# Optimization experiments

Measured on AMD Instinct MI355X. Metric: run time of the kernel, lower is better.

Reference implementation:

```python
import jax, jax.numpy as jnp
import numpy as np

N = 100000
E = 3200000
NFEAT, NHID, NCLASS = 512, 256, 64
K = 10
ALPHA = 0.1


def setup_inputs() -> dict:
    key = jax.random.key(0)
    k1, k2, k3, k4, k5 = jax.random.split(key, 5)
    x = jax.random.normal(k1, (N, NFEAT), dtype=jnp.float32)
    edge_index = jax.random.randint(k2, (2, E), 0, N, dtype=jnp.int64)
    # Linear params (Kaiming-ish scale)
    W1 = jax.random.normal(k3, (NFEAT, NHID), dtype=jnp.float32) / np.sqrt(NFEAT)
    b1 = jnp.zeros((NHID,), dtype=jnp.float32)
    W2 = jax.random.normal(k4, (NHID, NCLASS), dtype=jnp.float32) / np.sqrt(NHID)
    b2 = jnp.zeros((NCLASS,), dtype=jnp.float32)
    # GPR coefficients: temp[k] = alpha*(1-alpha)^k, temp[K] = (1-alpha)^K
    temp = ALPHA * (1.0 - ALPHA) ** np.arange(K + 1)
    temp[-1] = (1.0 - ALPHA) ** K
    temp = jnp.asarray(temp, dtype=jnp.float32)
    return {"x": x, "edge_index": edge_index, "W1": W1, "b1": b1,
            "W2": W2, "b2": b2, "temp": temp}


def _gcn_norm(edge_index, num_nodes):
    # add self-loops, symmetric GCN normalization (PyG gcn_norm, edge_weight=1)
    loop = jnp.arange(num_nodes, dtype=edge_index.dtype)
    src = jnp.concatenate([edge_index[0], loop])
    dst = jnp.concatenate([edge_index[1], loop])
    deg = jnp.zeros((num_nodes,), dtype=jnp.float32).at[dst].add(1.0)
    dinv = jnp.where(deg > 0, jax.lax.rsqrt(deg), 0.0)
    norm = dinv[src] * dinv[dst]
    return src, dst, norm


def reference(x, edge_index, W1, b1, W2, b2, temp):
    n = x.shape[0]
    # eval mode: dropout is identity
    h = jax.nn.relu(x @ W1 + b1)
    h = h @ W2 + b2  # [N, nclass]
    src, dst, norm = _gcn_norm(edge_index, n)
    hidden = h * temp[0]
    for k in range(K):
        # one GCN-normalized hop: out[dst] += norm * h[src]
        h = jax.ops.segment_sum(norm[:, None] * h[src], dst, num_segments=n)
        hidden = hidden + temp[k + 1] * h
    return jax.nn.log_softmax(hidden, axis=1)
```

## Files before the change

### kernel.cpp

```cpp
#include <hip/hip_runtime.h>

#define N_NODES 100000
#define N_EDGES 3200000
#define NFEAT 512
#define NHID 256
#define NCLASS 64
#define KHOPS 10
#define SCAN_B 391

#define NBSHIFT 9
#define NBUCK 196
#define BCAP 20480
#define TILE 4096

typedef __bf16 bf16x8 __attribute__((ext_vector_type(8)));
typedef __bf16 bf16x4 __attribute__((ext_vector_type(4)));
typedef float f32x4 __attribute__((ext_vector_type(4)));


__global__ __launch_bounds__(256) void zero_deg_kernel(int* __restrict__ deg, int* __restrict__ bcursor) {
    int i = blockIdx.x * 256 + threadIdx.x;
    if (i < N_NODES) deg[i] = 0;
    if (blockIdx.x == 0 && threadIdx.x < NBUCK) bcursor[threadIdx.x] = 0;
}

__global__ __launch_bounds__(256) void deg_kernel(const int* __restrict__ ei, int* __restrict__ deg) {
    int e = blockIdx.x * 256 + threadIdx.x;
    if (e < N_EDGES) atomicAdd(&deg[ei[N_EDGES + e]], 1);
}

__global__ __launch_bounds__(256) void dinv_kernel(const int* __restrict__ deg, float* __restrict__ dinv) {
    int i = blockIdx.x * 256 + threadIdx.x;
    if (i < N_NODES) dinv[i] = rsqrtf((float)(deg[i] + 1));
}


__global__ __launch_bounds__(256) void scan1_kernel(const int* __restrict__ deg, int* __restrict__ partial) {
    __shared__ int red[256];
    int t = threadIdx.x;
    int i = blockIdx.x * 256 + t;
    red[t] = (i < N_NODES) ? deg[i] + 1 : 0;
    __syncthreads();
    for (int off = 128; off > 0; off >>= 1) {
        if (t < off) red[t] += red[t + off];
        __syncthreads();
    }
    if (t == 0) partial[blockIdx.x] = red[0];
}

__global__ __launch_bounds__(512) void scan2_kernel(int* __restrict__ partial) {
    __shared__ int s[512];
    int t = threadIdx.x;
    int v = (t < SCAN_B) ? partial[t] : 0;
    s[t] = v;
    __syncthreads();
    for (int off = 1; off < 512; off <<= 1) {
        int add = (t >= off) ? s[t - off] : 0;
        __syncthreads();
        s[t] += add;
        __syncthreads();
    }
    if (t < SCAN_B) partial[t] = s[t] - v;
}

__global__ __launch_bounds__(256) void scan3_kernel(const int* __restrict__ deg,
                                                    const int* __restrict__ partial,
                                                    int* __restrict__ row_ptr,
                                                    int* __restrict__ cursor) {
    __shared__ int s[256];
    int t = threadIdx.x;
    int i = blockIdx.x * 256 + t;
    int v = (i < N_NODES) ? deg[i] + 1 : 0;
    s[t] = v;
    __syncthreads();
    for (int off = 1; off < 256; off <<= 1) {
        int add = (t >= off) ? s[t - off] : 0;
        __syncthreads();
        s[t] += add;
        __syncthreads();
    }
    int excl = s[t] - v + partial[blockIdx.x];
    if (i < N_NODES) {
        row_ptr[i] = excl;
        cursor[i] = excl;
        if (i == N_NODES - 1) row_ptr[N_NODES] = excl + v;
    }
}


__global__ __launch_bounds__(256) void radix1_kernel(const int* __restrict__ ei,
                                                     int* __restrict__ bcursor,
                                                     int2* __restrict__ breg) {
    __shared__ int2 stage[TILE];
    __shared__ int hist[NBUCK];
    __shared__ int base[NBUCK];
    __shared__ int offs[NBUCK];
    int t = threadIdx.x;
    int e0 = blockIdx.x * TILE;
    int n = N_EDGES - e0; if (n > TILE) n = TILE;
    for (int i = t; i < NBUCK; i += 256) { hist[i] = 0; offs[i] = 0; }
    __syncthreads();
    for (int i = t; i < n; i += 256) {
        int s = ei[e0 + i];
        int d = ei[N_EDGES + e0 + i];
        stage[i] = make_int2(s, d);
        atomicAdd(&hist[d >> NBSHIFT], 1);
    }
    __syncthreads();
    for (int i = t; i < NBUCK; i += 256)
        if (hist[i]) base[i] = atomicAdd(&bcursor[i], hist[i]);
    __syncthreads();
    for (int i = t; i < n; i += 256) {
        int2 e = stage[i];
        int b = e.y >> NBSHIFT;
        int slot = base[b] + atomicAdd(&offs[b], 1);
        if (slot < BCAP) breg[(size_t)b * BCAP + slot] = e;
    }
}


__global__ __launch_bounds__(256) void radix2_kernel(const int2* __restrict__ breg,
                                                     const int* __restrict__ bcursor,
                                                     const int* __restrict__ row_ptr,
                                                     int* __restrict__ esrc) {
    __shared__ int lcur[512];
    int b = blockIdx.x;
    int t = threadIdx.x;
    int d0 = b << NBSHIFT;
    int nn = N_NODES - d0; if (nn > 512) nn = 512;
    for (int j = t; j < nn; j += 256) {
        int rp = row_ptr[d0 + j];
        lcur[j] = rp + 1;
        esrc[rp] = d0 + j;
    }
    __syncthreads();
    int cnt = bcursor[b]; if (cnt > BCAP) cnt = BCAP;
    const int2* bp = breg + (size_t)b * BCAP;
    for (int i = t; i < cnt; i += 256) {
        int2 e = bp[i];
        int p = atomicAdd(&lcur[e.y - d0], 1);
        esrc[p] = e.x;
    }
}

__global__ __launch_bounds__(256) void fill_kernel(const int* __restrict__ ei,
                                                   int* __restrict__ cursor,
                                                   int* __restrict__ esrc) {
    int e = blockIdx.x * 256 + threadIdx.x;
    if (e < N_EDGES) {
        int s = ei[e], d = ei[N_EDGES + e];
        int p = atomicAdd(&cursor[d], 1);
        esrc[p] = s;
    } else if (e < N_EDGES + N_NODES) {
        int i = e - N_EDGES;
        int p = atomicAdd(&cursor[i], 1);
        esrc[p] = i;
    }
}


__global__ __launch_bounds__(256) void wprep_kernel(const float* __restrict__ W1,
                                                    const float* __restrict__ W2,
                                                    __bf16* __restrict__ w1t,
                                                    __bf16* __restrict__ w2t) {
    int i = blockIdx.x * 256 + threadIdx.x;
    if (i < NFEAT * NHID) {
        int n = i >> 9, k = i & 511;
        w1t[i] = (__bf16)W1[k * NHID + n];
    } else {
        int j = i - NFEAT * NHID;
        if (j < NHID * NCLASS) {
            int n = j >> 8, k = j & 255;
            w2t[j] = (__bf16)W2[k * NCLASS + n];
        }
    }
}


#define MT 64
#define KC 64
#define XP 72
#define WP 72
#define HP 264

__global__ __launch_bounds__(256) void mlp_kernel(const float* __restrict__ x,
                                                  const __bf16* __restrict__ w1t,
                                                  const float* __restrict__ b1,
                                                  const __bf16* __restrict__ w2t,
                                                  const float* __restrict__ b2,
                                                  const float* __restrict__ temp,
                                                  const float* __restrict__ dinv,
                                                  __bf16* __restrict__ u0,
                                                  float* __restrict__ hidden) {
    __shared__ char smem[46080] __attribute__((aligned(16)));
    __bf16* xs  = (__bf16*)smem;
    __bf16* wt  = (__bf16*)(smem + 9216);
    __bf16* h1s = (__bf16*)smem;

    int t = threadIdx.x;
    int wv = t >> 6, lane = t & 63;
    int lrow = lane & 15;
    int quad = lane >> 4;
    int row0 = blockIdx.x * MT;
    int n0 = wv * 64;

    f32x4 acc[4][4] = {};
    for (int kc = 0; kc < NFEAT; kc += KC) {
        __syncthreads();
        for (int i = t; i < MT * 16; i += 256) {
            int r = i >> 4, c4 = i & 15;
            int row = row0 + r; if (row >= N_NODES) row = N_NODES - 1;
            float4 v = *(const float4*)&x[(size_t)row * NFEAT + kc + c4 * 4];
            bf16x4 o = { (__bf16)v.x, (__bf16)v.y, (__bf16)v.z, (__bf16)v.w };
            *(bf16x4*)&xs[r * XP + c4 * 4] = o;
        }
        for (int i = t; i < 256 * 8; i += 256) {
            int n = i >> 3, c8 = i & 7;
            bf16x8 v = *(const bf16x8*)&w1t[(size_t)n * NFEAT + kc + c8 * 8];
            *(bf16x8*)&wt[n * WP + c8 * 8] = v;
        }
        __syncthreads();
        #pragma unroll
        for (int ks = 0; ks < 2; ++ks) {
            int kof = ks * 32 + quad * 8;
            bf16x8 a[4], b[4];
            #pragma unroll
            for (int mt = 0; mt < 4; ++mt)
                a[mt] = *(const bf16x8*)&xs[(mt * 16 + lrow) * XP + kof];
            #pragma unroll
            for (int nt = 0; nt < 4; ++nt)
                b[nt] = *(const bf16x8*)&wt[(n0 + nt * 16 + lrow) * WP + kof];
            #pragma unroll
            for (int mt = 0; mt < 4; ++mt)
                #pragma unroll
                for (int nt = 0; nt < 4; ++nt)
                    acc[mt][nt] = __builtin_amdgcn_mfma_f32_16x16x32_bf16(a[mt], b[nt], acc[mt][nt], 0, 0, 0);
        }
    }
    __syncthreads();
    #pragma unroll
    for (int nt = 0; nt < 4; ++nt) {
        int coln = n0 + nt * 16 + lrow;
        float bb = b1[coln];
        #pragma unroll
        for (int mt = 0; mt < 4; ++mt) {
            int rbase = mt * 16 + quad * 4;
            #pragma unroll
            for (int r = 0; r < 4; ++r) {
                float v = acc[mt][nt][r] + bb;
                h1s[(rbase + r) * HP + coln] = (__bf16)fmaxf(v, 0.f);
            }
        }
    }
    __syncthreads();
    f32x4 acc2[4] = {};
    #pragma unroll
    for (int ks = 0; ks < 8; ++ks) {
        int kof = ks * 32 + quad * 8;
        bf16x8 a2 = *(const bf16x8*)&h1s[(wv * 16 + lrow) * HP + kof];
        #pragma unroll
        for (int nt = 0; nt < 4; ++nt) {
            bf16x8 bv = *(const bf16x8*)&w2t[(size_t)(nt * 16 + lrow) * NHID + kof];
            acc2[nt] = __builtin_amdgcn_mfma_f32_16x16x32_bf16(a2, bv, acc2[nt], 0, 0, 0);
        }
    }
    float t0 = temp[0];
    #pragma unroll
    for (int nt = 0; nt < 4; ++nt) {
        int coln = nt * 16 + lrow;
        float bb = b2[coln];
        #pragma unroll
        for (int r = 0; r < 4; ++r) {
            int row = row0 + wv * 16 + quad * 4 + r;
            if (row < N_NODES) {
                float v = acc2[nt][r] + bb;
                size_t idx = (size_t)row * NCLASS + coln;
                hidden[idx] = t0 * v;
                u0[idx] = (__bf16)(dinv[row] * v);
            }
        }
    }
}


__global__ __launch_bounds__(256) void prop_kernel(const __bf16* __restrict__ uin,
                                                   __bf16* __restrict__ uout,
                                                   float* __restrict__ hidden,
                                                   const int* __restrict__ row_ptr,
                                                   const int* __restrict__ esrc,
                                                   const float* __restrict__ dinv,
                                                   const float* __restrict__ temp,
                                                   int ktap) {
    int node = blockIdx.x * 4 + (threadIdx.x >> 6);
    int lane = threadIdx.x & 63;
    int oct = lane >> 3, fi8 = lane & 7;
    int beg = row_ptr[node], end = row_ptr[node + 1];
    const uint4* urow = (const uint4*)uin;
    float acc[8] = {};
    int nit = (end - beg + 7) >> 3;
    #pragma unroll 4
    for (int it = 0; it < nit; ++it) {
        int e = beg + it * 8 + oct;
        int ec = min(e, end - 1);
        int s = __builtin_nontemporal_load(&esrc[ec]);
        float m = (e < end) ? 1.f : 0.f;
        uint4 v = urow[(size_t)s * 8 + fi8];
        unsigned vv;
        vv = v.x;
        acc[0] = fmaf(m, __int_as_float(vv << 16), acc[0]);
        acc[1] = fmaf(m, __int_as_float(vv & 0xffff0000u), acc[1]);
        vv = v.y;
        acc[2] = fmaf(m, __int_as_float(vv << 16), acc[2]);
        acc[3] = fmaf(m, __int_as_float(vv & 0xffff0000u), acc[3]);
        vv = v.z;
        acc[4] = fmaf(m, __int_as_float(vv << 16), acc[4]);
        acc[5] = fmaf(m, __int_as_float(vv & 0xffff0000u), acc[5]);
        vv = v.w;
        acc[6] = fmaf(m, __int_as_float(vv << 16), acc[6]);
        acc[7] = fmaf(m, __int_as_float(vv & 0xffff0000u), acc[7]);
    }
    #pragma unroll
    for (int j = 0; j < 8; ++j) {
        acc[j] += __shfl_xor(acc[j], 8);
        acc[j] += __shfl_xor(acc[j], 16);
        acc[j] += __shfl_xor(acc[j], 32);
    }
    if (oct == 0) {
        float di = dinv[node];
        float d2 = di * di;
        float tk = temp[ktap] * di;
        union { __bf16 b[8]; uint4 u; } pk;
        #pragma unroll
        for (int j = 0; j < 8; ++j) pk.b[j] = (__bf16)(d2 * acc[j]);
        ((uint4*)uout)[(size_t)node * 8 + fi8] = pk.u;
        float* hp = hidden + (size_t)node * NCLASS + fi8 * 8;
        float4 a = *(float4*)hp, b = *(float4*)(hp + 4);
        a.x = fmaf(tk, acc[0], a.x); a.y = fmaf(tk, acc[1], a.y);
        a.z = fmaf(tk, acc[2], a.z); a.w = fmaf(tk, acc[3], a.w);
        b.x = fmaf(tk, acc[4], b.x); b.y = fmaf(tk, acc[5], b.y);
        b.z = fmaf(tk, acc[6], b.z); b.w = fmaf(tk, acc[7], b.w);
        *(float4*)hp = a; *(float4*)(hp + 4) = b;
    }
}


__global__ __launch_bounds__(256) void lsm_kernel(float* __restrict__ io) {
    int i = blockIdx.x * 4 + (threadIdx.x >> 6);
    int j = threadIdx.x & 63;
    float v = io[(size_t)i * 64 + j];
    float m = v;
    #pragma unroll
    for (int o = 32; o > 0; o >>= 1) m = fmaxf(m, __shfl_xor(m, o));
    float ex = expf(v - m);
    float s = ex;
    #pragma unroll
    for (int o = 32; o > 0; o >>= 1) s += __shfl_xor(s, o);
    io[(size_t)i * 64 + j] = v - m - logf(s);
}

extern "C" void kernel_launch(void* const* d_in, const int* in_sizes, int n_in,
                              void* d_out, int out_size, void* d_ws, size_t ws_size,
                              hipStream_t stream) {
    const float* x    = (const float*)d_in[0];
    const int*   ei   = (const int*)d_in[1];
    const float* W1   = (const float*)d_in[2];
    const float* b1   = (const float*)d_in[3];
    const float* W2   = (const float*)d_in[4];
    const float* b2   = (const float*)d_in[5];
    const float* temp = (const float*)d_in[6];
    float* out = (float*)d_out;

    char* ws = (char*)d_ws;
    size_t off = 0;
    auto alloc = [&](size_t bytes) -> void* {
        void* p = ws + off;
        off = (off + bytes + 255) & ~(size_t)255;
        return p;
    };
    int*    deg     = (int*)alloc((size_t)N_NODES * 4);
    float*  dinv    = (float*)alloc((size_t)N_NODES * 4);
    int*    row_ptr = (int*)alloc((size_t)(N_NODES + 1) * 4);
    int*    cursor  = (int*)alloc((size_t)N_NODES * 4);
    int*    partial = (int*)alloc((size_t)SCAN_B * 4);
    int*    bcursor = (int*)alloc((size_t)NBUCK * 4);
    int*    esrc    = (int*)alloc((size_t)(N_EDGES + N_NODES) * 4);
    __bf16* ub0     = (__bf16*)alloc((size_t)N_NODES * NCLASS * 2);
    __bf16* ub1     = (__bf16*)alloc((size_t)N_NODES * NCLASS * 2);
    __bf16* w1t     = (__bf16*)alloc((size_t)NFEAT * NHID * 2);
    __bf16* w2t     = (__bf16*)alloc((size_t)NHID * NCLASS * 2);
    size_t breg_bytes = (size_t)NBUCK * BCAP * 8;
    bool use_radix = (off + breg_bytes <= ws_size);
    int2* breg = use_radix ? (int2*)alloc(breg_bytes) : (int2*)0;

    zero_deg_kernel<<<(N_NODES + 255) / 256, 256, 0, stream>>>(deg, bcursor);
    deg_kernel<<<(N_EDGES + 255) / 256, 256, 0, stream>>>(ei, deg);
    dinv_kernel<<<(N_NODES + 255) / 256, 256, 0, stream>>>(deg, dinv);
    scan1_kernel<<<SCAN_B, 256, 0, stream>>>(deg, partial);
    scan2_kernel<<<1, 512, 0, stream>>>(partial);
    scan3_kernel<<<SCAN_B, 256, 0, stream>>>(deg, partial, row_ptr, cursor);
    if (use_radix) {
        radix1_kernel<<<(N_EDGES + TILE - 1) / TILE, 256, 0, stream>>>(ei, bcursor, breg);
        radix2_kernel<<<NBUCK, 256, 0, stream>>>(breg, bcursor, row_ptr, esrc);
    } else {
        fill_kernel<<<(N_EDGES + N_NODES + 255) / 256, 256, 0, stream>>>(ei, cursor, esrc);
    }
    wprep_kernel<<<(NFEAT * NHID + NHID * NCLASS + 255) / 256, 256, 0, stream>>>(W1, W2, w1t, w2t);

    mlp_kernel<<<(N_NODES + MT - 1) / MT, 256, 0, stream>>>(x, w1t, b1, w2t, b2, temp, dinv, ub0, out);

    __bf16* cur = ub0;
    __bf16* nxt = ub1;
    for (int k = 0; k < KHOPS; ++k) {
        prop_kernel<<<N_NODES / 4, 256, 0, stream>>>(cur, nxt, out, row_ptr, esrc, dinv, temp, k + 1);
        __bf16* tswap = cur; cur = nxt; nxt = tswap;
    }

    lsm_kernel<<<N_NODES / 4, 256, 0, stream>>>(out);
}
```

Baseline: 1.238 ms.

## Split propagation features into two halves and load MLP operands directly from global

The propagated bf16 features are stored as two separate 32-column planes, and each hop launches a 2D grid that processes one half per block. Each plane's working set is half as large, which should fit better in cache during the random gathers, at the cost of reading the edge lists twice and doing one more shuffle stage. The MLP kernel also drops its LDS staging of x and W1 and loads MFMA operands straight from global memory, which removes the barriers but gives up LDS reuse and coalesced loads.

```diff
diff --git a/kernel.cpp b/kernel.cpp
--- a/kernel.cpp
+++ b/kernel.cpp
@@ -178,9 +178,6 @@
 
 
 #define MT 64
-#define KC 64
-#define XP 72
-#define WP 72
 #define HP 264
 
 __global__ __launch_bounds__(256) void mlp_kernel(const float* __restrict__ x,
@@ -192,10 +189,7 @@
                                                   const float* __restrict__ dinv,
                                                   __bf16* __restrict__ u0,
                                                   float* __restrict__ hidden) {
-    __shared__ char smem[46080] __attribute__((aligned(16)));
-    __bf16* xs  = (__bf16*)smem;
-    __bf16* wt  = (__bf16*)(smem + 9216);
-    __bf16* h1s = (__bf16*)smem;
+    __shared__ __bf16 h1s[MT * HP];
 
     int t = threadIdx.x;
     int wv = t >> 6, lane = t & 63;
@@ -204,32 +198,31 @@
     int row0 = blockIdx.x * MT;
     int n0 = wv * 64;
 
+    int arow[4];
+    #pragma unroll
+    for (int mt = 0; mt < 4; ++mt) {
+        int r = row0 + mt * 16 + lrow;
+        arow[mt] = (r < N_NODES) ? r : (N_NODES - 1);
+    }
+
     f32x4 acc[4][4] = {};
-    for (int kc = 0; kc < NFEAT; kc += KC) {
-        __syncthreads();
-        for (int i = t; i < MT * 16; i += 256) {
-            int r = i >> 4, c4 = i & 15;
-            int row = row0 + r; if (row >= N_NODES) row = N_NODES - 1;
-            float4 v = *(const float4*)&x[(size_t)row * NFEAT + kc + c4 * 4];
-            bf16x4 o = { (__bf16)v.x, (__bf16)v.y, (__bf16)v.z, (__bf16)v.w };
-            *(bf16x4*)&xs[r * XP + c4 * 4] = o;
-        }
-        for (int i = t; i < 256 * 8; i += 256) {
-            int n = i >> 3, c8 = i & 7;
-            bf16x8 v = *(const bf16x8*)&w1t[(size_t)n * NFEAT + kc + c8 * 8];
-            *(bf16x8*)&wt[n * WP + c8 * 8] = v;
-        }
-        __syncthreads();
+    #pragma unroll 1
+    for (int kc = 0; kc < NFEAT; kc += 64) {
         #pragma unroll
         for (int ks = 0; ks < 2; ++ks) {
-            int kof = ks * 32 + quad * 8;
+            int kof = kc + ks * 32 + quad * 8;
             bf16x8 a[4], b[4];
             #pragma unroll
-            for (int mt = 0; mt < 4; ++mt)
-                a[mt] = *(const bf16x8*)&xs[(mt * 16 + lrow) * XP + kof];
+            for (int mt = 0; mt < 4; ++mt) {
+                const float* xp = &x[(size_t)arow[mt] * NFEAT + kof];
+                float4 v0 = *(const float4*)xp;
+                float4 v1 = *(const float4*)(xp + 4);
+                a[mt] = (bf16x8){ (__bf16)v0.x, (__bf16)v0.y, (__bf16)v0.z, (__bf16)v0.w,
+                                  (__bf16)v1.x, (__bf16)v1.y, (__bf16)v1.z, (__bf16)v1.w };
+            }
             #pragma unroll
             for (int nt = 0; nt < 4; ++nt)
-                b[nt] = *(const bf16x8*)&wt[(n0 + nt * 16 + lrow) * WP + kof];
+                b[nt] = *(const bf16x8*)&w1t[(size_t)(n0 + nt * 16 + lrow) * NFEAT + kof];
             #pragma unroll
             for (int mt = 0; mt < 4; ++mt)
                 #pragma unroll
@@ -237,7 +230,6 @@
                     acc[mt][nt] = __builtin_amdgcn_mfma_f32_16x16x32_bf16(a[mt], b[nt], acc[mt][nt], 0, 0, 0);
         }
     }
-    __syncthreads();
     #pragma unroll
     for (int nt = 0; nt < 4; ++nt) {
         int coln = n0 + nt * 16 + lrow;
@@ -269,14 +261,14 @@
     for (int nt = 0; nt < 4; ++nt) {
         int coln = nt * 16 + lrow;
         float bb = b2[coln];
+        int hlf = coln >> 5, cin = coln & 31;
         #pragma unroll
         for (int r = 0; r < 4; ++r) {
             int row = row0 + wv * 16 + quad * 4 + r;
             if (row < N_NODES) {
                 float v = acc2[nt][r] + bb;
-                size_t idx = (size_t)row * NCLASS + coln;
-                hidden[idx] = t0 * v;
-                u0[idx] = (__bf16)(dinv[row] * v);
+                hidden[(size_t)row * NCLASS + coln] = t0 * v;
+                u0[((size_t)hlf * N_NODES + row) * 32 + cin] = (__bf16)(dinv[row] * v);
             }
         }
     }
@@ -291,20 +283,21 @@
                                                    const float* __restrict__ dinv,
                                                    const float* __restrict__ temp,
                                                    int ktap) {
+    int half = blockIdx.y;
     int node = blockIdx.x * 4 + (threadIdx.x >> 6);
     int lane = threadIdx.x & 63;
-    int oct = lane >> 3, fi8 = lane & 7;
+    int eslot = lane >> 2, fi = lane & 3;
     int beg = row_ptr[node], end = row_ptr[node + 1];
-    const uint4* urow = (const uint4*)uin;
+    const uint4* ub = (const uint4*)(uin + (size_t)half * N_NODES * 32);
     float acc[8] = {};
-    int nit = (end - beg + 7) >> 3;
-    #pragma unroll 4
+    int nit = (end - beg + 15) >> 4;
+    #pragma unroll 2
     for (int it = 0; it < nit; ++it) {
-        int e = beg + it * 8 + oct;
+        int e = beg + it * 16 + eslot;
         int ec = min(e, end - 1);
         int s = __builtin_nontemporal_load(&esrc[ec]);
         float m = (e < end) ? 1.f : 0.f;
-        uint4 v = urow[(size_t)s * 8 + fi8];
+        uint4 v = ub[(size_t)s * 4 + fi];
         unsigned vv;
         vv = v.x;
         acc[0] = fmaf(m, __int_as_float(vv << 16), acc[0]);
@@ -321,19 +314,20 @@
     }
     #pragma unroll
     for (int j = 0; j < 8; ++j) {
+        acc[j] += __shfl_xor(acc[j], 4);
         acc[j] += __shfl_xor(acc[j], 8);
         acc[j] += __shfl_xor(acc[j], 16);
         acc[j] += __shfl_xor(acc[j], 32);
     }
-    if (oct == 0) {
+    if (eslot == 0) {
         float di = dinv[node];
         float d2 = di * di;
         float tk = temp[ktap] * di;
         union { __bf16 b[8]; uint4 u; } pk;
         #pragma unroll
         for (int j = 0; j < 8; ++j) pk.b[j] = (__bf16)(d2 * acc[j]);
-        ((uint4*)uout)[(size_t)node * 8 + fi8] = pk.u;
-        float* hp = hidden + (size_t)node * NCLASS + fi8 * 8;
+        ((uint4*)(uout + (size_t)half * N_NODES * 32))[(size_t)node * 4 + fi] = pk.u;
+        float* hp = hidden + (size_t)node * NCLASS + half * 32 + fi * 8;
         float4 a = *(float4*)hp, b = *(float4*)(hp + 4);
         a.x = fmaf(tk, acc[0], a.x); a.y = fmaf(tk, acc[1], a.y);
         a.z = fmaf(tk, acc[2], a.z); a.w = fmaf(tk, acc[3], a.w);
@@ -410,8 +404,9 @@
 
     __bf16* cur = ub0;
     __bf16* nxt = ub1;
+    dim3 pgrid(N_NODES / 4, 2);
     for (int k = 0; k < KHOPS; ++k) {
-        prop_kernel<<<N_NODES / 4, 256, 0, stream>>>(cur, nxt, out, row_ptr, esrc, dinv, temp, k + 1);
+        prop_kernel<<<pgrid, 256, 0, stream>>>(cur, nxt, out, row_ptr, esrc, dinv, temp, k + 1);
         __bf16* tswap = cur; cur = nxt; nxt = tswap;
     }
 
```

New measurement: 1.613 ms. 30.3% more time.

## Load MLP operands directly from global into registers, halve row tile

Applied to the files above, without the earlier changes.

The first MLP GEMM no longer stages x and W1 tiles through shared memory with per-chunk barriers. Each lane now loads its MFMA fragments straight from global memory, converting x to bf16 in registers and prefetching the next k-step's x values into a double buffer. The row tile drops from 64 to 32, so there are twice as many blocks and less shared memory per block, and the second GEMM is re-split across waves as 2x2 row/column groups. This removes LDS traffic and barriers, but W1 is now read from global/L2 by every block with less reuse per load, and the x reads are strided rather than coalesced.

```diff
diff --git a/kernel.cpp b/kernel.cpp
--- a/kernel.cpp
+++ b/kernel.cpp
@@ -177,11 +177,38 @@
 }
 
 
-#define MT 64
-#define KC 64
-#define XP 72
-#define WP 72
+#define MT 32
 #define HP 264
+
+__device__ __forceinline__ bf16x8 cvt8(const float4& v0, const float4& v1) {
+    return (bf16x8){ (__bf16)v0.x, (__bf16)v0.y, (__bf16)v0.z, (__bf16)v0.w,
+                     (__bf16)v1.x, (__bf16)v1.y, (__bf16)v1.z, (__bf16)v1.w };
+}
+
+__device__ __forceinline__ void mlp_step(const float* xr0, const float* xr1,
+                                         const __bf16* wr0, const __bf16* wr1,
+                                         const __bf16* wr2, const __bf16* wr3,
+                                         float4 (&avc)[2][2], float4 (&avn)[2][2],
+                                         f32x4 (&acc)[2][4], int kcur, int knext) {
+    avn[0][0] = *(const float4*)(xr0 + knext);
+    avn[0][1] = *(const float4*)(xr0 + knext + 4);
+    avn[1][0] = *(const float4*)(xr1 + knext);
+    avn[1][1] = *(const float4*)(xr1 + knext + 4);
+    bf16x8 b0 = *(const bf16x8*)(wr0 + kcur);
+    bf16x8 b1 = *(const bf16x8*)(wr1 + kcur);
+    bf16x8 b2 = *(const bf16x8*)(wr2 + kcur);
+    bf16x8 b3 = *(const bf16x8*)(wr3 + kcur);
+    bf16x8 a0 = cvt8(avc[0][0], avc[0][1]);
+    bf16x8 a1 = cvt8(avc[1][0], avc[1][1]);
+    acc[0][0] = __builtin_amdgcn_mfma_f32_16x16x32_bf16(a0, b0, acc[0][0], 0, 0, 0);
+    acc[0][1] = __builtin_amdgcn_mfma_f32_16x16x32_bf16(a0, b1, acc[0][1], 0, 0, 0);
+    acc[0][2] = __builtin_amdgcn_mfma_f32_16x16x32_bf16(a0, b2, acc[0][2], 0, 0, 0);
+    acc[0][3] = __builtin_amdgcn_mfma_f32_16x16x32_bf16(a0, b3, acc[0][3], 0, 0, 0);
+    acc[1][0] = __builtin_amdgcn_mfma_f32_16x16x32_bf16(a1, b0, acc[1][0], 0, 0, 0);
+    acc[1][1] = __builtin_amdgcn_mfma_f32_16x16x32_bf16(a1, b1, acc[1][1], 0, 0, 0);
+    acc[1][2] = __builtin_amdgcn_mfma_f32_16x16x32_bf16(a1, b2, acc[1][2], 0, 0, 0);
+    acc[1][3] = __builtin_amdgcn_mfma_f32_16x16x32_bf16(a1, b3, acc[1][3], 0, 0, 0);
+}
 
 __global__ __launch_bounds__(256) void mlp_kernel(const float* __restrict__ x,
                                                   const __bf16* __restrict__ w1t,
@@ -192,10 +219,7 @@
                                                   const float* __restrict__ dinv,
                                                   __bf16* __restrict__ u0,
                                                   float* __restrict__ hidden) {
-    __shared__ char smem[46080] __attribute__((aligned(16)));
-    __bf16* xs  = (__bf16*)smem;
-    __bf16* wt  = (__bf16*)(smem + 9216);
-    __bf16* h1s = (__bf16*)smem;
+    __shared__ __bf16 h1s[MT * HP];
 
     int t = threadIdx.x;
     int wv = t >> 6, lane = t & 63;
@@ -204,46 +228,34 @@
     int row0 = blockIdx.x * MT;
     int n0 = wv * 64;
 
-    f32x4 acc[4][4] = {};
-    for (int kc = 0; kc < NFEAT; kc += KC) {
-        __syncthreads();
-        for (int i = t; i < MT * 16; i += 256) {
-            int r = i >> 4, c4 = i & 15;
-            int row = row0 + r; if (row >= N_NODES) row = N_NODES - 1;
-            float4 v = *(const float4*)&x[(size_t)row * NFEAT + kc + c4 * 4];
-            bf16x4 o = { (__bf16)v.x, (__bf16)v.y, (__bf16)v.z, (__bf16)v.w };
-            *(bf16x4*)&xs[r * XP + c4 * 4] = o;
-        }
-        for (int i = t; i < 256 * 8; i += 256) {
-            int n = i >> 3, c8 = i & 7;
-            bf16x8 v = *(const bf16x8*)&w1t[(size_t)n * NFEAT + kc + c8 * 8];
-            *(bf16x8*)&wt[n * WP + c8 * 8] = v;
-        }
-        __syncthreads();
-        #pragma unroll
-        for (int ks = 0; ks < 2; ++ks) {
-            int kof = ks * 32 + quad * 8;
-            bf16x8 a[4], b[4];
-            #pragma unroll
-            for (int mt = 0; mt < 4; ++mt)
-                a[mt] = *(const bf16x8*)&xs[(mt * 16 + lrow) * XP + kof];
-            #pragma unroll
-            for (int nt = 0; nt < 4; ++nt)
-                b[nt] = *(const bf16x8*)&wt[(n0 + nt * 16 + lrow) * WP + kof];
-            #pragma unroll
-            for (int mt = 0; mt < 4; ++mt)
-                #pragma unroll
-                for (int nt = 0; nt < 4; ++nt)
-                    acc[mt][nt] = __builtin_amdgcn_mfma_f32_16x16x32_bf16(a[mt], b[nt], acc[mt][nt], 0, 0, 0);
-        }
-    }
-    __syncthreads();
+    int r0 = row0 + lrow;      if (r0 >= N_NODES) r0 = N_NODES - 1;
+    int r1 = row0 + 16 + lrow; if (r1 >= N_NODES) r1 = N_NODES - 1;
+    const float* xr0 = &x[(size_t)r0 * NFEAT + quad * 8];
+    const float* xr1 = &x[(size_t)r1 * NFEAT + quad * 8];
+    const __bf16* wr0 = &w1t[(size_t)(n0 +  0 + lrow) * NFEAT + quad * 8];
+    const __bf16* wr1 = &w1t[(size_t)(n0 + 16 + lrow) * NFEAT + quad * 8];
+    const __bf16* wr2 = &w1t[(size_t)(n0 + 32 + lrow) * NFEAT + quad * 8];
+    const __bf16* wr3 = &w1t[(size_t)(n0 + 48 + lrow) * NFEAT + quad * 8];
+
+    float4 av0[2][2], av1[2][2];
+    av0[0][0] = *(const float4*)xr0; av0[0][1] = *(const float4*)(xr0 + 4);
+    av0[1][0] = *(const float4*)xr1; av0[1][1] = *(const float4*)(xr1 + 4);
+
+    f32x4 acc[2][4] = {};
+    #pragma unroll
+    for (int ks = 0; ks < 16; ks += 2) {
+        mlp_step(xr0, xr1, wr0, wr1, wr2, wr3, av0, av1, acc,
+                 ks * 32, ((ks + 1) & 15) * 32);
+        mlp_step(xr0, xr1, wr0, wr1, wr2, wr3, av1, av0, acc,
+                 (ks + 1) * 32, ((ks + 2) & 15) * 32);
+    }
+
     #pragma unroll
     for (int nt = 0; nt < 4; ++nt) {
         int coln = n0 + nt * 16 + lrow;
         float bb = b1[coln];
         #pragma unroll
-        for (int mt = 0; mt < 4; ++mt) {
+        for (int mt = 0; mt < 2; ++mt) {
             int rbase = mt * 16 + quad * 4;
             #pragma unroll
             for (int r = 0; r < 4; ++r) {
@@ -253,25 +265,28 @@
         }
     }
     __syncthreads();
-    f32x4 acc2[4] = {};
+
+    int rg = (wv >> 1) * 16;
+    int cg = (wv & 1) * 32;
+    f32x4 acc2[2] = {};
     #pragma unroll
     for (int ks = 0; ks < 8; ++ks) {
         int kof = ks * 32 + quad * 8;
-        bf16x8 a2 = *(const bf16x8*)&h1s[(wv * 16 + lrow) * HP + kof];
+        bf16x8 a2 = *(const bf16x8*)&h1s[(rg + lrow) * HP + kof];
         #pragma unroll
-        for (int nt = 0; nt < 4; ++nt) {
-            bf16x8 bv = *(const bf16x8*)&w2t[(size_t)(nt * 16 + lrow) * NHID + kof];
+        for (int nt = 0; nt < 2; ++nt) {
+            bf16x8 bv = *(const bf16x8*)&w2t[(size_t)(cg + nt * 16 + lrow) * NHID + kof];
             acc2[nt] = __builtin_amdgcn_mfma_f32_16x16x32_bf16(a2, bv, acc2[nt], 0, 0, 0);
         }
     }
     float t0 = temp[0];
     #pragma unroll
-    for (int nt = 0; nt < 4; ++nt) {
-        int coln = nt * 16 + lrow;
+    for (int nt = 0; nt < 2; ++nt) {
+        int coln = cg + nt * 16 + lrow;
         float bb = b2[coln];
         #pragma unroll
         for (int r = 0; r < 4; ++r) {
-            int row = row0 + wv * 16 + quad * 4 + r;
+            int row = row0 + rg + quad * 4 + r;
             if (row < N_NODES) {
                 float v = acc2[nt][r] + bb;
                 size_t idx = (size_t)row * NCLASS + coln;
```

Result: slower. 1.284 ms (+3.7%).

## Enlarge MLP tile to 128 rows with 512 threads and register-prefetch x

Applied to the files above, without the earlier changes.

The MLP kernel now handles 128 rows per block with 8 waves in a 2x4 wave grid, so each W1 chunk loaded into shared memory is reused across twice as many rows. The x chunk for the next K step is loaded into registers while the MFMA work for the current step runs, hiding global load latency. The second GEMM is redistributed so each wave computes a 32x32 output tile. Shared memory per block grows to about 66 KB, and with launch_bounds(512,4) this may limit occupancy or cause register spills.

```diff
diff --git a/kernel.cpp b/kernel.cpp
--- a/kernel.cpp
+++ b/kernel.cpp
@@ -177,24 +177,24 @@
 }
 
 
-#define MT 64
+#define MT 128
 #define KC 64
 #define XP 72
 #define WP 72
 #define HP 264
 
-__global__ __launch_bounds__(256) void mlp_kernel(const float* __restrict__ x,
-                                                  const __bf16* __restrict__ w1t,
-                                                  const float* __restrict__ b1,
-                                                  const __bf16* __restrict__ w2t,
-                                                  const float* __restrict__ b2,
-                                                  const float* __restrict__ temp,
-                                                  const float* __restrict__ dinv,
-                                                  __bf16* __restrict__ u0,
-                                                  float* __restrict__ hidden) {
-    __shared__ char smem[46080] __attribute__((aligned(16)));
+__global__ __launch_bounds__(512, 4) void mlp_kernel(const float* __restrict__ x,
+                                                     const __bf16* __restrict__ w1t,
+                                                     const float* __restrict__ b1,
+                                                     const __bf16* __restrict__ w2t,
+                                                     const float* __restrict__ b2,
+                                                     const float* __restrict__ temp,
+                                                     const float* __restrict__ dinv,
+                                                     __bf16* __restrict__ u0,
+                                                     float* __restrict__ hidden) {
+    __shared__ char smem[67584] __attribute__((aligned(16)));
     __bf16* xs  = (__bf16*)smem;
-    __bf16* wt  = (__bf16*)(smem + 9216);
+    __bf16* wt  = (__bf16*)(smem + 18432);
     __bf16* h1s = (__bf16*)smem;
 
     int t = threadIdx.x;
@@ -202,34 +202,59 @@
     int lrow = lane & 15;
     int quad = lane >> 4;
     int row0 = blockIdx.x * MT;
-    int n0 = wv * 64;
+    int wm = (wv >> 2) * 64;
+    int wn = (wv & 3) * 64;
+
+    const float* xpt[2];
+    int xr[2], xc8[2];
+    #pragma unroll
+    for (int it = 0; it < 2; ++it) {
+        int j = it * 512 + t;
+        int r = j >> 3, c8 = j & 7;
+        int rr = row0 + r; if (rr >= N_NODES) rr = N_NODES - 1;
+        xpt[it] = &x[(size_t)rr * NFEAT + c8 * 8];
+        xr[it] = r; xc8[it] = c8;
+    }
+    float4 px[4];
+    px[0] = *(const float4*)(xpt[0]);
+    px[1] = *(const float4*)(xpt[0] + 4);
+    px[2] = *(const float4*)(xpt[1]);
+    px[3] = *(const float4*)(xpt[1] + 4);
 
     f32x4 acc[4][4] = {};
+    #pragma unroll 1
     for (int kc = 0; kc < NFEAT; kc += KC) {
         __syncthreads();
-        for (int i = t; i < MT * 16; i += 256) {
-            int r = i >> 4, c4 = i & 15;
-            int row = row0 + r; if (row >= N_NODES) row = N_NODES - 1;
-            float4 v = *(const float4*)&x[(size_t)row * NFEAT + kc + c4 * 4];
-            bf16x4 o = { (__bf16)v.x, (__bf16)v.y, (__bf16)v.z, (__bf16)v.w };
-            *(bf16x4*)&xs[r * XP + c4 * 4] = o;
-        }
-        for (int i = t; i < 256 * 8; i += 256) {
-            int n = i >> 3, c8 = i & 7;
-            bf16x8 v = *(const bf16x8*)&w1t[(size_t)n * NFEAT + kc + c8 * 8];
-            *(bf16x8*)&wt[n * WP + c8 * 8] = v;
-        }
-        __syncthreads();
+        #pragma unroll
+        for (int it = 0; it < 2; ++it) {
+            float4 v0 = px[it * 2], v1 = px[it * 2 + 1];
+            bf16x8 o = { (__bf16)v0.x, (__bf16)v0.y, (__bf16)v0.z, (__bf16)v0.w,
+                         (__bf16)v1.x, (__bf16)v1.y, (__bf16)v1.z, (__bf16)v1.w };
+            *(bf16x8*)&xs[xr[it] * XP + xc8[it] * 8] = o;
+        }
+        #pragma unroll
+        for (int it = 0; it < 4; ++it) {
+            int j = it * 512 + t;
+            int n = j >> 3, c8 = j & 7;
+            *(bf16x8*)&wt[n * WP + c8 * 8] = *(const bf16x8*)&w1t[(size_t)n * NFEAT + kc + c8 * 8];
+        }
+        __syncthreads();
+        if (kc + KC < NFEAT) {
+            px[0] = *(const float4*)(xpt[0] + kc + KC);
+            px[1] = *(const float4*)(xpt[0] + kc + KC + 4);
+            px[2] = *(const float4*)(xpt[1] + kc + KC);
+            px[3] = *(const float4*)(xpt[1] + kc + KC + 4);
+        }
         #pragma unroll
         for (int ks = 0; ks < 2; ++ks) {
             int kof = ks * 32 + quad * 8;
             bf16x8 a[4], b[4];
             #pragma unroll
             for (int mt = 0; mt < 4; ++mt)
-                a[mt] = *(const bf16x8*)&xs[(mt * 16 + lrow) * XP + kof];
+                a[mt] = *(const bf16x8*)&xs[(wm + mt * 16 + lrow) * XP + kof];
             #pragma unroll
             for (int nt = 0; nt < 4; ++nt)
-                b[nt] = *(const bf16x8*)&wt[(n0 + nt * 16 + lrow) * WP + kof];
+                b[nt] = *(const bf16x8*)&wt[(wn + nt * 16 + lrow) * WP + kof];
             #pragma unroll
             for (int mt = 0; mt < 4; ++mt)
                 #pragma unroll
@@ -240,11 +265,11 @@
     __syncthreads();
     #pragma unroll
     for (int nt = 0; nt < 4; ++nt) {
-        int coln = n0 + nt * 16 + lrow;
+        int coln = wn + nt * 16 + lrow;
         float bb = b1[coln];
         #pragma unroll
         for (int mt = 0; mt < 4; ++mt) {
-            int rbase = mt * 16 + quad * 4;
+            int rbase = wm + mt * 16 + quad * 4;
             #pragma unroll
             for (int r = 0; r < 4; ++r) {
                 float v = acc[mt][nt][r] + bb;
@@ -253,30 +278,41 @@
         }
     }
     __syncthreads();
-    f32x4 acc2[4] = {};
+    int rg = (wv >> 1) * 32;
+    int cg = (wv & 1) * 32;
+    f32x4 acc2[2][2] = {};
     #pragma unroll
     for (int ks = 0; ks < 8; ++ks) {
         int kof = ks * 32 + quad * 8;
-        bf16x8 a2 = *(const bf16x8*)&h1s[(wv * 16 + lrow) * HP + kof];
-        #pragma unroll
-        for (int nt = 0; nt < 4; ++nt) {
-            bf16x8 bv = *(const bf16x8*)&w2t[(size_t)(nt * 16 + lrow) * NHID + kof];
-            acc2[nt] = __builtin_amdgcn_mfma_f32_16x16x32_bf16(a2, bv, acc2[nt], 0, 0, 0);
-        }
+        bf16x8 a2[2], bv[2];
+        #pragma unroll
+        for (int m2 = 0; m2 < 2; ++m2)
+            a2[m2] = *(const bf16x8*)&h1s[(rg + m2 * 16 + lrow) * HP + kof];
+        #pragma unroll
+        for (int nt = 0; nt < 2; ++nt)
+            bv[nt] = *(const bf16x8*)&w2t[(size_t)(cg + nt * 16 + lrow) * NHID + kof];
+        #pragma unroll
+        for (int m2 = 0; m2 < 2; ++m2)
+            #pragma unroll
+            for (int nt = 0; nt < 2; ++nt)
+                acc2[m2][nt] = __builtin_amdgcn_mfma_f32_16x16x32_bf16(a2[m2], bv[nt], acc2[m2][nt], 0, 0, 0);
     }
     float t0 = temp[0];
     #pragma unroll
-    for (int nt = 0; nt < 4; ++nt) {
-        int coln = nt * 16 + lrow;
-        float bb = b2[coln];
-        #pragma unroll
-        for (int r = 0; r < 4; ++r) {
-            int row = row0 + wv * 16 + quad * 4 + r;
-            if (row < N_NODES) {
-                float v = acc2[nt][r] + bb;
-                size_t idx = (size_t)row * NCLASS + coln;
-                hidden[idx] = t0 * v;
-                u0[idx] = (__bf16)(dinv[row] * v);
+    for (int m2 = 0; m2 < 2; ++m2) {
+        #pragma unroll
+        for (int nt = 0; nt < 2; ++nt) {
+            int coln = cg + nt * 16 + lrow;
+            float bb = b2[coln];
+            #pragma unroll
+            for (int r = 0; r < 4; ++r) {
+                int row = row0 + rg + m2 * 16 + quad * 4 + r;
+                if (row < N_NODES) {
+                    float v = acc2[m2][nt][r] + bb;
+                    size_t idx = (size_t)row * NCLASS + coln;
+                    hidden[idx] = t0 * v;
+                    u0[idx] = (__bf16)(dinv[row] * v);
+                }
             }
         }
     }
@@ -406,7 +442,7 @@
     }
     wprep_kernel<<<(NFEAT * NHID + NHID * NCLASS + 255) / 256, 256, 0, stream>>>(W1, W2, w1t, w2t);
 
-    mlp_kernel<<<(N_NODES + MT - 1) / MT, 256, 0, stream>>>(x, w1t, b1, w2t, b2, temp, dinv, ub0, out);
+    mlp_kernel<<<(N_NODES + MT - 1) / MT, 512, 0, stream>>>(x, w1t, b1, w2t, b2, temp, dinv, ub0, out);
 
     __bf16* cur = ub0;
     __bf16* nxt = ub1;
```

Result: faster. 1.165 ms (-5.9%).
